# Optimization experiments

Measured on AMD Instinct MI355X. Metric: run time of the kernel, lower is better.

The kernel has to match this reference:

```python
import jax, jax.numpy as jnp
import numpy as np

X_DIM = 20000   # number of input locations (x_l rows)
Y_DIM = 6000    # number of query locations (y_l rows)
REGION_DEG = 10.0  # lon/lat spread so every query has neighbors within 250 km
EARTH_DIAM = 2.0 * 6.378  # thousand-km diameter used by the source
THRESH = 0.25   # 250 km neighborhood threshold


def setup_inputs() -> dict:
    key = jax.random.key(0)
    k1, k2, k3 = jax.random.split(key, 3)
    x = jax.random.normal(k1, (X_DIM, 1), dtype=jnp.float32)
    x_l = jax.random.uniform(k2, (X_DIM, 2), dtype=jnp.float32) * REGION_DEG
    y_l = jax.random.uniform(k3, (Y_DIM, 2), dtype=jnp.float32) * REGION_DEG
    return {"x": x, "x_l": x_l, "y_l": y_l}


def reference(x, x_l, y_l):
    # Training branch of GPR.call, vectorized over the y_dim python loop.
    d2r = jnp.pi / 180.0
    lon_x, lat_x = x_l[:, 0], x_l[:, 1]   # (X,)
    lon_y, lat_y = y_l[:, 0], y_l[:, 1]   # (Y,)
    # haversine terms, shape (Y, X)
    hav = jnp.sin((lat_x[None, :] - lat_y[:, None]) * d2r) ** 2
    hav = hav + (jnp.cos(lat_x * d2r)[None, :] * jnp.cos(lat_y * d2r)[:, None]
                 * jnp.sin((lon_x[None, :] - lon_y[:, None]) * d2r) ** 2)
    d = EARTH_DIAM * jnp.arcsin(jnp.sqrt(hav))  # great-circle distance (thousand km)
    # threshold + gather/scatter in source == masked weights here
    w = jnp.where(d < THRESH, d, 0.0)
    s = jnp.sum(w, axis=1, keepdims=True)        # (Y, 1) per-row normalizer
    L = jnp.where(s > 0, w / jnp.maximum(s, 1e-12), 0.0)  # (Y, X) sparse-ish weights
    m = (L @ x)[:, 0]                            # (Y,) squeezed mean
    # V = 0.001 * I  (noise=None path); returned value is diag_part(V)
    v_diag = jnp.full((y_l.shape[0],), 0.001, dtype=x.dtype)
    return m, v_diag
```

## Files before the change

### kernel.cpp

```cpp
#include <hip/hip_runtime.h>
#include <math.h>


#define TPB    256
#define YPB    4
#define NSTRIP 40
#define NLON   40
#define NCELLS (NSTRIP * NLON)
#define C_CELL   0.25f
#define INV_CELL 4.0f
#define RLAT     1.1250f

__device__ __forceinline__ float sin_poly(float a) {
    float t = a * a;
    return a * fmaf(t, fmaf(t, 8.3333333e-3f, -0.16666667f), 1.0f);
}
__device__ __forceinline__ float cos_poly(float a) {
    float t = a * a;
    return fmaf(t, fmaf(t, fmaf(t, -1.3888889e-3f, 4.1666668e-2f), -0.5f), 1.0f);
}
__device__ __forceinline__ int cell_of(float lon, float lat) {
    int s = (int)(lat * INV_CELL); s = min(max(s, 0), NSTRIP - 1);
    int l = (int)(lon * INV_CELL); l = min(max(l, 0), NLON - 1);
    return s * NLON + l;
}


__global__ __launch_bounds__(TPB) void zero_kernel(int* __restrict__ hist) {
    for (int i = threadIdx.x; i < NCELLS; i += TPB) hist[i] = 0;
}

__global__ __launch_bounds__(TPB) void hist_kernel(
    const float* __restrict__ x_l, int* __restrict__ hist, int nx)
{
    int i = blockIdx.x * TPB + threadIdx.x;
    if (i < nx) atomicAdd(&hist[cell_of(x_l[2 * i], x_l[2 * i + 1])], 1);
}

__global__ __launch_bounds__(TPB) void scan_kernel(
    const int* __restrict__ hist, int* __restrict__ cellStart,
    int* __restrict__ cursor)
{
    const int CHUNK = (NCELLS + TPB - 1) / TPB;
    __shared__ int sums[TPB];
    int tid = threadIdx.x;
    int base = tid * CHUNK;
    int local[7];
    int s = 0;
    #pragma unroll
    for (int j = 0; j < CHUNK; ++j) {
        int idx = base + j;
        int v = (idx < NCELLS) ? hist[idx] : 0;
        local[j] = s; s += v;
    }
    sums[tid] = s;
    __syncthreads();
    for (int off = 1; off < TPB; off <<= 1) {
        int t = (tid >= off) ? sums[tid - off] : 0;
        __syncthreads();
        sums[tid] += t;
        __syncthreads();
    }
    int excl = (tid > 0) ? sums[tid - 1] : 0;
    #pragma unroll
    for (int j = 0; j < CHUNK; ++j) {
        int idx = base + j;
        if (idx < NCELLS) { cellStart[idx] = excl + local[j]; cursor[idx] = excl + local[j]; }
    }
    if (tid == TPB - 1) cellStart[NCELLS] = sums[TPB - 1];
}

__global__ __launch_bounds__(TPB) void scatter_kernel(
    const float* __restrict__ x, const float* __restrict__ x_l,
    int* __restrict__ cursor, float4* __restrict__ sortedA,
    float2* __restrict__ sortedRaw, float* __restrict__ sortedX, int nx)
{
    const float d2r = 0.017453292519943295f;
    int i = blockIdx.x * TPB + threadIdx.x;
    if (i < nx) {
        float lon = x_l[2 * i], lat = x_l[2 * i + 1];
        int pos = atomicAdd(&cursor[cell_of(lon, lat)], 1);
        float al = lat * d2r, ao = lon * d2r;
        sortedA[pos]   = make_float4(sin_poly(al), cos_poly(al),
                                     sin_poly(ao), cos_poly(ao));
        sortedRaw[pos] = make_float2(lon, lat);
        sortedX[pos]   = x[i];
    }
}


__global__ __launch_bounds__(TPB) void gpr_binned(
    const float4* __restrict__ sortedA,
    const float2* __restrict__ sortedRaw,
    const float*  __restrict__ sortedX,
    const int*    __restrict__ cellStart,
    const float*  __restrict__ y_l,
    float* __restrict__ out, int ny, float Hcut, float HcutM)
{
    const int tid  = threadIdx.x;
    const int wave = tid >> 6;
    const int lane = tid & 63;
    const int y    = blockIdx.x * YPB + wave;

    const float d2r    = 0.017453292519943295f;
    const float r2d    = 57.29577951308232f;
    const float THRESH = 0.25f;
    const float DIAM   = 12.756f;
    const float DIAM6  = 12.756f / 6.0f;
    const float EPS_H  = 5e-8f;

    float lon_y = 0.0f, lat_y = 0.0f;
    if (y < ny) { lon_y = y_l[2 * y]; lat_y = y_l[2 * y + 1]; }
    const float sly   = sin_poly(lat_y * d2r);
    const float cly   = cos_poly(lat_y * d2r);
    const float slony = sin_poly(lon_y * d2r);
    const float clony = cos_poly(lon_y * d2r);

    float accw = 0.0f, accwx = 0.0f;

    const int s0 = max(0,          (int)floorf((lat_y - RLAT) * INV_CELL));
    const int s1 = min(NSTRIP - 1, (int)floorf((lat_y + RLAT) * INV_CELL));

    for (int s = s0; s <= s1; ++s) {
        float slo = s * C_CELL, shi = slo + C_CELL;
        float dmin = fmaxf(0.0f, fmaxf(slo - lat_y, lat_y - shi));
        float de   = fmaxf(0.0f, dmin - 3e-3f);
        float sd_  = sin_poly(de * d2r);
        float rem  = HcutM - sd_ * sd_;
        if (rem <= 0.0f) continue;
        float ccm = cos_poly(fminf(shi, 10.0f) * d2r) * cly * 0.999999f;
        float W   = asinf(fminf(1.0f, sqrtf(rem / ccm))) * r2d + 4e-3f;
        int lo = min(NLON - 1, max(0, (int)floorf((lon_y - W) * INV_CELL)));
        int hi = min(NLON - 1, max(0, (int)floorf((lon_y + W) * INV_CELL)));
        int p0 = cellStart[s * NLON + lo];
        int p1 = cellStart[s * NLON + hi + 1];

        for (int k = p0 + lane; k < p1; k += 64) {
            float4 e  = sortedA[k];
            float  xv = sortedX[k];

            float sl  = fmaf(e.x, cly,   -(e.y * sly));
            float sd  = fmaf(e.z, clony, -(e.w * slony));
            float cxy = e.y * cly;
            float hav = fmaf(sl, sl, cxy * (sd * sd));

            float tb  = hav - Hcut;
            float r   = __builtin_amdgcn_sqrtf(hav);
            float d   = r * fmaf(hav, DIAM6, DIAM);

            float w;
            if (__builtin_expect(fabsf(tb) < EPS_H, 0)) {
                float2 raw = sortedRaw[k];
                float lonx = raw.x, latx = raw.y;

                float dlat = __fsub_rn(latx, lat_y);
                float alat = __fmul_rn(dlat, d2r);
                float slf  = (float)sin((double)alat);
                float h1   = __fmul_rn(slf, slf);

                float axl  = __fmul_rn(latx,  d2r);
                float ayl  = __fmul_rn(lat_y, d2r);
                float cxf  = (float)cos((double)axl);
                float cyf  = (float)cos((double)ayl);
                float cc   = __fmul_rn(cxf, cyf);

                float dlon = __fsub_rn(lonx, lon_y);
                float alon = __fmul_rn(dlon, d2r);
                float sdf  = (float)sin((double)alon);
                float h2   = __fmul_rn(sdf, sdf);

                float hv   = __fadd_rn(h1, __fmul_rn(cc, h2));
                float r32  = (float)sqrt((double)hv);
                float as32 = (float)asin((double)r32);
                float dnp  = __fmul_rn(DIAM, as32);
                w = (dnp < THRESH) ? dnp : 0.0f;
            } else {
                w = (tb < 0.0f) ? d : 0.0f;
            }

            accw += w;
            accwx = fmaf(w, xv, accwx);
        }
    }

    #pragma unroll
    for (int off = 32; off > 0; off >>= 1) {
        accw  += __shfl_xor(accw,  off, 64);
        accwx += __shfl_xor(accwx, off, 64);
    }

    if (lane == 0 && y < ny) {
        float m = (accw > 0.0f) ? (accwx / fmaxf(accw, 1e-12f)) : 0.0f;
        out[y]      = m;
        out[ny + y] = 0.001f;
    }
}


__global__ __launch_bounds__(TPB) void gpr_full(
    const float* __restrict__ x, const float* __restrict__ x_l,
    const float* __restrict__ y_l, float* __restrict__ out,
    int nx, int ny, float Hcut)
{
    __shared__ float4 tA[1024];
    __shared__ float  tX[1024];

    const int tid  = threadIdx.x;
    const int wave = tid >> 6;
    const int lane = tid & 63;
    const int y    = blockIdx.x * YPB + wave;

    const float d2r    = 0.017453292519943295f;
    const float THRESH = 0.25f;
    const float DIAM   = 12.756f;
    const float DIAM6  = 12.756f / 6.0f;
    const float EPS_H  = 5e-8f;

    float lon_y = 0.0f, lat_y = 0.0f;
    if (y < ny) { lon_y = y_l[2 * y]; lat_y = y_l[2 * y + 1]; }
    const float sly   = sin_poly(lat_y * d2r);
    const float cly   = cos_poly(lat_y * d2r);
    const float slony = sin_poly(lon_y * d2r);
    const float clony = cos_poly(lon_y * d2r);

    float accw = 0.0f, accwx = 0.0f;

    const int ntiles = (nx + 1023) / 1024;
    for (int t = 0; t < ntiles; ++t) {
        const int base = t * 1024;
        __syncthreads();
        #pragma unroll
        for (int j = 0; j < 1024 / TPB; ++j) {
            int idx = j * TPB + tid, i = base + idx;
            if (i < nx) {
                float lon = x_l[2 * i], lat = x_l[2 * i + 1];
                tA[idx] = make_float4(sin_poly(lat * d2r), cos_poly(lat * d2r),
                                      sin_poly(lon * d2r), cos_poly(lon * d2r));
                tX[idx] = x[i];
            }
        }
        __syncthreads();

        const int tn = min(1024, nx - base);
        for (int k = lane; k < tn; k += 64) {
            float4 e  = tA[k];
            float  xv = tX[k];
            float sl  = fmaf(e.x, cly,   -(e.y * sly));
            float sd  = fmaf(e.z, clony, -(e.w * slony));
            float cxy = e.y * cly;
            float hav = fmaf(sl, sl, cxy * (sd * sd));
            float tb  = hav - Hcut;
            float r   = __builtin_amdgcn_sqrtf(hav);
            float d   = r * fmaf(hav, DIAM6, DIAM);
            float w;
            if (__builtin_expect(fabsf(tb) < EPS_H, 0)) {
                int   i    = base + k;
                float lonx = x_l[2 * i], latx = x_l[2 * i + 1];
                float dlat = __fsub_rn(latx, lat_y);
                float alat = __fmul_rn(dlat, d2r);
                float slf  = (float)sin((double)alat);
                float h1   = __fmul_rn(slf, slf);
                float axl  = __fmul_rn(latx,  d2r);
                float ayl  = __fmul_rn(lat_y, d2r);
                float cxf  = (float)cos((double)axl);
                float cyf  = (float)cos((double)ayl);
                float cc   = __fmul_rn(cxf, cyf);
                float dlon = __fsub_rn(lonx, lon_y);
                float alon = __fmul_rn(dlon, d2r);
                float sdf  = (float)sin((double)alon);
                float h2   = __fmul_rn(sdf, sdf);
                float hv   = __fadd_rn(h1, __fmul_rn(cc, h2));
                float r32  = (float)sqrt((double)hv);
                float as32 = (float)asin((double)r32);
                float dnp  = __fmul_rn(DIAM, as32);
                w = (dnp < THRESH) ? dnp : 0.0f;
            } else {
                w = (tb < 0.0f) ? d : 0.0f;
            }
            accw += w;
            accwx = fmaf(w, xv, accwx);
        }
    }

    #pragma unroll
    for (int off = 32; off > 0; off >>= 1) {
        accw  += __shfl_xor(accw,  off, 64);
        accwx += __shfl_xor(accwx, off, 64);
    }

    if (lane == 0 && y < ny) {
        float m = (accw > 0.0f) ? (accwx / fmaxf(accw, 1e-12f)) : 0.0f;
        out[y]      = m;
        out[ny + y] = 0.001f;
    }
}


extern "C" void kernel_launch(void* const* d_in, const int* in_sizes, int n_in,
                              void* d_out, int out_size, void* d_ws, size_t ws_size,
                              hipStream_t stream) {
    const float* x   = (const float*)d_in[0];
    const float* x_l = (const float*)d_in[1];
    const float* y_l = (const float*)d_in[2];
    float* out = (float*)d_out;

    const int nx = in_sizes[0];
    const int ny = in_sizes[2] / 2;

    double th = 0.25 / 12.756;
    double s  = sin(th);
    float Hcut  = (float)(s * s);
    float HcutM = (float)(s * s * 1.001);

    size_t offA   = 0;
    size_t offRaw = offA   + (size_t)nx * sizeof(float4);
    size_t offX   = offRaw + (size_t)nx * sizeof(float2);
    size_t offH   = offX   + (size_t)nx * sizeof(float);
    size_t offCS  = offH   + (size_t)NCELLS * sizeof(int);
    size_t offCur = (offCS + (size_t)(NCELLS + 1) * sizeof(int) + 15) & ~(size_t)15;
    size_t total  = offCur + (size_t)NCELLS * sizeof(int);

    const int blocks = (ny + YPB - 1) / YPB;

    if (ws_size >= total) {
        float4* sortedA   = (float4*)((char*)d_ws + offA);
        float2* sortedRaw = (float2*)((char*)d_ws + offRaw);
        float*  sortedX   = (float*) ((char*)d_ws + offX);
        int*    hist      = (int*)   ((char*)d_ws + offH);
        int*    cellStart = (int*)   ((char*)d_ws + offCS);
        int*    cursor    = (int*)   ((char*)d_ws + offCur);

        int xb = (nx + TPB - 1) / TPB;
        zero_kernel<<<1, TPB, 0, stream>>>(hist);
        hist_kernel<<<xb, TPB, 0, stream>>>(x_l, hist, nx);
        scan_kernel<<<1, TPB, 0, stream>>>(hist, cellStart, cursor);
        scatter_kernel<<<xb, TPB, 0, stream>>>(x, x_l, cursor,
                                               sortedA, sortedRaw, sortedX, nx);
        gpr_binned<<<blocks, TPB, 0, stream>>>(sortedA, sortedRaw, sortedX,
                                               cellStart, y_l, out,
                                               ny, Hcut, HcutM);
    } else {
        gpr_full<<<blocks, TPB, 0, stream>>>(x, x_l, y_l, out, nx, ny, Hcut);
    }
}
```

Baseline: 93.73 us.

## Sort query points by grid cell so neighboring waves share candidate bins

Query points are now binned into the same spatial grid as the inputs, using a histogram, scan and scatter pass, and processed in cell order. Waves in the same block and adjacent blocks therefore visit the same input cells, which should improve cache locality in the binned gather. Each result is written back through the original query index. The cost is extra preprocessing work, workspace for the sorted query arrays, and scattered output writes.

```diff
diff --git a/kernel.cpp b/kernel.cpp
--- a/kernel.cpp
+++ b/kernel.cpp
@@ -26,23 +26,35 @@
 }
 
 
-__global__ __launch_bounds__(TPB) void zero_kernel(int* __restrict__ hist) {
-    for (int i = threadIdx.x; i < NCELLS; i += TPB) hist[i] = 0;
+__global__ __launch_bounds__(TPB) void zero_kernel(int* __restrict__ histX,
+                                                   int* __restrict__ histY) {
+    for (int i = threadIdx.x; i < NCELLS; i += TPB) { histX[i] = 0; histY[i] = 0; }
 }
 
 __global__ __launch_bounds__(TPB) void hist_kernel(
-    const float* __restrict__ x_l, int* __restrict__ hist, int nx)
+    const float* __restrict__ x_l, const float* __restrict__ y_l,
+    int* __restrict__ histX, int* __restrict__ histY, int nx, int ny)
 {
     int i = blockIdx.x * TPB + threadIdx.x;
-    if (i < nx) atomicAdd(&hist[cell_of(x_l[2 * i], x_l[2 * i + 1])], 1);
+    if (i < nx) {
+        atomicAdd(&histX[cell_of(x_l[2 * i], x_l[2 * i + 1])], 1);
+    } else if (i < nx + ny) {
+        int j = i - nx;
+        atomicAdd(&histY[cell_of(y_l[2 * j], y_l[2 * j + 1])], 1);
+    }
 }
 
 __global__ __launch_bounds__(TPB) void scan_kernel(
-    const int* __restrict__ hist, int* __restrict__ cellStart,
-    int* __restrict__ cursor)
+    const int* __restrict__ histX, const int* __restrict__ histY,
+    int* __restrict__ csX, int* __restrict__ csY,
+    int* __restrict__ curX, int* __restrict__ curY)
 {
     const int CHUNK = (NCELLS + TPB - 1) / TPB;
     __shared__ int sums[TPB];
+    const int* hist      = (blockIdx.x == 0) ? histX : histY;
+    int*       cellStart = (blockIdx.x == 0) ? csX  : csY;
+    int*       cursor    = (blockIdx.x == 0) ? curX : curY;
+
     int tid = threadIdx.x;
     int base = tid * CHUNK;
     int local[7];
@@ -72,19 +84,29 @@
 
 __global__ __launch_bounds__(TPB) void scatter_kernel(
     const float* __restrict__ x, const float* __restrict__ x_l,
-    int* __restrict__ cursor, float4* __restrict__ sortedA,
-    float2* __restrict__ sortedRaw, float* __restrict__ sortedX, int nx)
+    const float* __restrict__ y_l,
+    int* __restrict__ curX, int* __restrict__ curY,
+    float4* __restrict__ sortedA, float2* __restrict__ sortedRaw,
+    float*  __restrict__ sortedX,
+    float2* __restrict__ sortedYL, int* __restrict__ sortedYIdx,
+    int nx, int ny)
 {
     const float d2r = 0.017453292519943295f;
     int i = blockIdx.x * TPB + threadIdx.x;
     if (i < nx) {
         float lon = x_l[2 * i], lat = x_l[2 * i + 1];
-        int pos = atomicAdd(&cursor[cell_of(lon, lat)], 1);
+        int pos = atomicAdd(&curX[cell_of(lon, lat)], 1);
         float al = lat * d2r, ao = lon * d2r;
         sortedA[pos]   = make_float4(sin_poly(al), cos_poly(al),
                                      sin_poly(ao), cos_poly(ao));
         sortedRaw[pos] = make_float2(lon, lat);
         sortedX[pos]   = x[i];
+    } else if (i < nx + ny) {
+        int j = i - nx;
+        float lon = y_l[2 * j], lat = y_l[2 * j + 1];
+        int pos = atomicAdd(&curY[cell_of(lon, lat)], 1);
+        sortedYL[pos]   = make_float2(lon, lat);
+        sortedYIdx[pos] = j;
     }
 }
 
@@ -94,13 +116,14 @@
     const float2* __restrict__ sortedRaw,
     const float*  __restrict__ sortedX,
     const int*    __restrict__ cellStart,
-    const float*  __restrict__ y_l,
+    const float2* __restrict__ sortedYL,
+    const int*    __restrict__ sortedYIdx,
     float* __restrict__ out, int ny, float Hcut, float HcutM)
 {
     const int tid  = threadIdx.x;
     const int wave = tid >> 6;
     const int lane = tid & 63;
-    const int y    = blockIdx.x * YPB + wave;
+    const int j    = blockIdx.x * YPB + wave;
 
     const float d2r    = 0.017453292519943295f;
     const float r2d    = 57.29577951308232f;
@@ -109,8 +132,13 @@
     const float DIAM6  = 12.756f / 6.0f;
     const float EPS_H  = 5e-8f;
 
+    int   yidx  = 0;
     float lon_y = 0.0f, lat_y = 0.0f;
-    if (y < ny) { lon_y = y_l[2 * y]; lat_y = y_l[2 * y + 1]; }
+    if (j < ny) {
+        yidx = sortedYIdx[j];
+        float2 p = sortedYL[j];
+        lon_y = p.x; lat_y = p.y;
+    }
     const float sly   = sin_poly(lat_y * d2r);
     const float cly   = cos_poly(lat_y * d2r);
     const float slony = sin_poly(lon_y * d2r);
@@ -189,10 +217,10 @@
         accwx += __shfl_xor(accwx, off, 64);
     }
 
-    if (lane == 0 && y < ny) {
+    if (lane == 0 && j < ny) {
         float m = (accw > 0.0f) ? (accwx / fmaxf(accw, 1e-12f)) : 0.0f;
-        out[y]      = m;
-        out[ny + y] = 0.001f;
+        out[yidx]      = m;
+        out[ny + yidx] = 0.001f;
     }
 }
 
@@ -230,8 +258,8 @@
         const int base = t * 1024;
         __syncthreads();
         #pragma unroll
-        for (int j = 0; j < 1024 / TPB; ++j) {
-            int idx = j * TPB + tid, i = base + idx;
+        for (int jj = 0; jj < 1024 / TPB; ++jj) {
+            int idx = jj * TPB + tid, i = base + idx;
             if (i < nx) {
                 float lon = x_l[2 * i], lat = x_l[2 * i + 1];
                 tA[idx] = make_float4(sin_poly(lat * d2r), cos_poly(lat * d2r),
@@ -314,31 +342,42 @@
 
     size_t offA   = 0;
     size_t offRaw = offA   + (size_t)nx * sizeof(float4);
-    size_t offX   = offRaw + (size_t)nx * sizeof(float2);
-    size_t offH   = offX   + (size_t)nx * sizeof(float);
-    size_t offCS  = offH   + (size_t)NCELLS * sizeof(int);
-    size_t offCur = (offCS + (size_t)(NCELLS + 1) * sizeof(int) + 15) & ~(size_t)15;
-    size_t total  = offCur + (size_t)NCELLS * sizeof(int);
+    size_t offYL  = offRaw + (size_t)nx * sizeof(float2);
+    size_t offX   = offYL  + (size_t)ny * sizeof(float2);
+    size_t offYI  = offX   + (size_t)nx * sizeof(float);
+    size_t offHX  = offYI  + (size_t)ny * sizeof(int);
+    size_t offHY  = offHX  + (size_t)NCELLS * sizeof(int);
+    size_t offCSX = offHY  + (size_t)NCELLS * sizeof(int);
+    size_t offCSY = offCSX + (size_t)(NCELLS + 1) * sizeof(int);
+    size_t offCuX = offCSY + (size_t)(NCELLS + 1) * sizeof(int);
+    size_t offCuY = offCuX + (size_t)NCELLS * sizeof(int);
+    size_t total  = offCuY + (size_t)NCELLS * sizeof(int);
 
     const int blocks = (ny + YPB - 1) / YPB;
 
     if (ws_size >= total) {
-        float4* sortedA   = (float4*)((char*)d_ws + offA);
-        float2* sortedRaw = (float2*)((char*)d_ws + offRaw);
-        float*  sortedX   = (float*) ((char*)d_ws + offX);
-        int*    hist      = (int*)   ((char*)d_ws + offH);
-        int*    cellStart = (int*)   ((char*)d_ws + offCS);
-        int*    cursor    = (int*)   ((char*)d_ws + offCur);
-
-        int xb = (nx + TPB - 1) / TPB;
-        zero_kernel<<<1, TPB, 0, stream>>>(hist);
-        hist_kernel<<<xb, TPB, 0, stream>>>(x_l, hist, nx);
-        scan_kernel<<<1, TPB, 0, stream>>>(hist, cellStart, cursor);
-        scatter_kernel<<<xb, TPB, 0, stream>>>(x, x_l, cursor,
-                                               sortedA, sortedRaw, sortedX, nx);
+        float4* sortedA    = (float4*)((char*)d_ws + offA);
+        float2* sortedRaw  = (float2*)((char*)d_ws + offRaw);
+        float2* sortedYL   = (float2*)((char*)d_ws + offYL);
+        float*  sortedX    = (float*) ((char*)d_ws + offX);
+        int*    sortedYIdx = (int*)   ((char*)d_ws + offYI);
+        int*    histX      = (int*)   ((char*)d_ws + offHX);
+        int*    histY      = (int*)   ((char*)d_ws + offHY);
+        int*    csX        = (int*)   ((char*)d_ws + offCSX);
+        int*    csY        = (int*)   ((char*)d_ws + offCSY);
+        int*    curX       = (int*)   ((char*)d_ws + offCuX);
+        int*    curY       = (int*)   ((char*)d_ws + offCuY);
+
+        int nb = (nx + ny + TPB - 1) / TPB;
+        zero_kernel<<<1, TPB, 0, stream>>>(histX, histY);
+        hist_kernel<<<nb, TPB, 0, stream>>>(x_l, y_l, histX, histY, nx, ny);
+        scan_kernel<<<2, TPB, 0, stream>>>(histX, histY, csX, csY, curX, curY);
+        scatter_kernel<<<nb, TPB, 0, stream>>>(x, x_l, y_l, curX, curY,
+                                               sortedA, sortedRaw, sortedX,
+                                               sortedYL, sortedYIdx, nx, ny);
         gpr_binned<<<blocks, TPB, 0, stream>>>(sortedA, sortedRaw, sortedX,
-                                               cellStart, y_l, out,
-                                               ny, Hcut, HcutM);
+                                               csX, sortedYL, sortedYIdx,
+                                               out, ny, Hcut, HcutM);
     } else {
         gpr_full<<<blocks, TPB, 0, stream>>>(x, x_l, y_l, out, nx, ny, Hcut);
     }
```

After: 91.37 us. -2.5%, faster.
